# Optimization experiments

Hardware: AMD Instinct MI355X
Metric: run time of the kernel (lower is better)

Reference implementation:

```python
import jax, jax.numpy as jnp
import numpy as np

N_GRAPHS = 4
NODES_PER_GRAPH = 8192
N_NODES = N_GRAPHS * NODES_PER_GRAPH
N_EDGES = N_NODES * 16
IN_DIM = 3
HID = 128
K_OUT = 512
MAX_WAVELENGTH = 10000.0


def _glorot(k, shape):
    lim = (6.0 / (shape[0] + shape[1])) ** 0.5
    return jax.random.uniform(k, shape, jnp.float32, -lim, lim)


def setup_inputs() -> dict:
    key = jax.random.key(0)
    ks = jax.random.split(key, 12)
    z = lambda *s: jnp.zeros(s, jnp.float32)
    return {
        "x": jax.random.normal(ks[0], (N_NODES, IN_DIM), jnp.float32),
        "mesh_pos": jax.random.uniform(ks[1], (N_NODES, 2), jnp.float32),
        "mesh_edges": jax.random.randint(ks[2], (N_EDGES, 2), 0, N_NODES, jnp.int32),
        "batch_idx": jnp.arange(N_NODES, dtype=jnp.int32) // NODES_PER_GRAPH,
        "proj_w": _glorot(ks[3], (IN_DIM, HID)), "proj_b": z(HID),
        "msg_w1": _glorot(ks[4], (2 * HID, HID)), "msg_b1": z(HID),
        "msg_w2": _glorot(ks[5], (HID, HID)), "msg_b2": z(HID),
        "upd_w1": _glorot(ks[6], (2 * HID, HID)), "upd_b1": z(HID),
        "upd_w2": _glorot(ks[7], (HID, HID)), "upd_b2": z(HID),
        "pool_rel_w": _glorot(ks[8], (HID, 1)), "pool_rel_b": z(1),
        "pool_root_w": _glorot(ks[9], (HID, 1)),
    }


def _sincos_embed(pos):
    # ContinuousSincosEmbed: HID=128, ndim=2 -> 64 channels per coord dim, 32 freqs
    dim_per_ndim = HID // 2
    omega = 1.0 / MAX_WAVELENGTH ** (jnp.arange(0, dim_per_ndim, 2, dtype=jnp.float32) / dim_per_ndim)
    ang = pos[:, :, None] * omega  # [N, ndim, 32]
    emb = jnp.concatenate([jnp.sin(ang), jnp.cos(ang)], axis=-1)  # [N, ndim, 64]
    return emb.reshape(pos.shape[0], HID)


def reference(x, mesh_pos, mesh_edges, batch_idx, proj_w, proj_b,
              msg_w1, msg_b1, msg_w2, msg_b2, upd_w1, upd_b1, upd_w2, upd_b2,
              pool_rel_w, pool_rel_b, pool_root_w):
    src, dst = mesh_edges[:, 0], mesh_edges[:, 1]  # edge_index[0]=j(src), [1]=i(dst)
    h = x @ proj_w + proj_b + _sincos_embed(mesh_pos)
    cnt = jnp.maximum(jax.ops.segment_sum(jnp.ones((N_EDGES,), h.dtype), dst, num_segments=N_NODES), 1.0)
    # message passing layer (depth=1): message MLP on [x_i, x_j], scatter-mean, residual update MLP
    m_in = jnp.concatenate([h[dst], h[src]], axis=-1)  # [E, 2H]
    m = jax.nn.silu(m_in @ msg_w1 + msg_b1) @ msg_w2 + msg_b2
    agg = jax.ops.segment_sum(m, dst, num_segments=N_NODES) / cnt[:, None]
    h = h + (jax.nn.silu(jnp.concatenate([h, agg], axis=-1) @ upd_w1 + upd_b1) @ upd_w2 + upd_b2)
    # SAGPooling score: GraphConv(HID,1,aggr='mean'), tanh nonlinearity
    nagg = jax.ops.segment_sum(h[src], dst, num_segments=N_NODES) / cnt[:, None]
    score = jnp.tanh((nagg @ pool_rel_w + pool_rel_b + h @ pool_root_w)[:, 0])
    # fixed top-k per graph (batch_idx is contiguous blocks of NODES_PER_GRAPH)
    topv, topi = jax.lax.top_k(score.reshape(N_GRAPHS, NODES_PER_GRAPH), K_OUT)
    perm = (topi + jnp.arange(N_GRAPHS, dtype=topi.dtype)[:, None] * NODES_PER_GRAPH).reshape(-1)
    x_pool = h[perm] * topv.reshape(-1)[:, None]
    batch_pool = jnp.repeat(jnp.arange(N_GRAPHS, dtype=batch_idx.dtype), K_OUT)
    return x_pool, batch_pool
```

## Files before the change

kernel.cpp:

```cpp
#include <hip/hip_runtime.h>
#include <hip/hip_bf16.h>
#include <math.h>

#define N_NODESC 32768
#define N_EDGESC 524288
#define NPG 8192
#define KOUT 512

typedef unsigned short u16;
typedef unsigned int u32;
typedef unsigned long long u64;

__device__ __forceinline__ float siluf(float x) {
    return x / (1.f + __expf(-x));
}

__global__ __launch_bounds__(256) void k_h0(const float* __restrict__ x,
                                            const float* __restrict__ pos,
                                            const float* __restrict__ pw,
                                            const float* __restrict__ pb,
                                            float* __restrict__ h,
                                            int* __restrict__ deg) {
    int gid = blockIdx.x * 256 + threadIdx.x;
    if (gid < N_NODESC) deg[gid] = 0;
    int node = blockIdx.x * 2 + (threadIdx.x >> 7);
    int c = threadIdx.x & 127;
    float x0 = x[node * 3 + 0];
    float x1 = x[node * 3 + 1];
    float x2 = x[node * 3 + 2];
    float acc = x0 * pw[c] + x1 * pw[128 + c] + x2 * pw[256 + c];
    acc += pb[c];
    int dim = c >> 6;
    int inner = c & 63;
    int jj = inner & 31;
    float p = pos[node * 2 + dim];
    float omega = exp2f(-(float)jj * 0.41524101186092027f);
    float ang = p * omega;
    acc += (inner < 32) ? __sinf(ang) : __cosf(ang);
    h[(size_t)node * 128 + c] = acc;
}

__global__ __launch_bounds__(256) void k_deg(const int* __restrict__ edges, int* __restrict__ deg) {
    int e = blockIdx.x * 256 + threadIdx.x;
    if (e < N_EDGESC) {
        int2 e2 = ((const int2*)edges)[e];
        atomicAdd(&deg[e2.y], 1);
    }
}

__global__ __launch_bounds__(1024) void k_scan(const int* __restrict__ deg,
                                               int* __restrict__ off, int* __restrict__ cur,
                                               float* __restrict__ rs, float* __restrict__ bg) {
    __shared__ int ls[1024];
    int tid = threadIdx.x;
    int base = tid * 32;
    int v[32];
    int s = 0;
#pragma unroll
    for (int j = 0; j < 32; j++) { v[j] = deg[base + j]; s += v[j]; }
    ls[tid] = s;
    __syncthreads();
    for (int ofs = 1; ofs < 1024; ofs <<= 1) {
        int t = (tid >= ofs) ? ls[tid - ofs] : 0;
        __syncthreads();
        ls[tid] += t;
        __syncthreads();
    }
    int run = ls[tid] - s;
#pragma unroll
    for (int j = 0; j < 32; j++) {
        off[base + j] = run;
        cur[base + j] = run;
        int d = v[j];
        rs[base + j] = 1.f / (float)(d > 0 ? d : 1);
        bg[base + j] = d > 0 ? 1.f : 0.f;
        run += d;
    }
}

__global__ __launch_bounds__(256) void k_fill(const int* __restrict__ edges,
                                              int* __restrict__ cur, int* __restrict__ csr) {
    int e = blockIdx.x * 256 + threadIdx.x;
    if (e < N_EDGESC) {
        int2 e2 = ((const int2*)edges)[e];
        int pos = atomicAdd(&cur[e2.y], 1);
        csr[pos] = e2.x;
    }
}

__global__ __launch_bounds__(256) void k_sortcsr(int* __restrict__ csr,
                                                 const int* __restrict__ off,
                                                 const int* __restrict__ deg) {
    int d = blockIdx.x * 4 + (threadIdx.x >> 6);
    int lane = threadIdx.x & 63;
    int o = off[d], n = deg[d];
    if (n <= 1) return;
    if (n <= 64) {
        int key = (lane < n) ? csr[o + lane] : 0x7FFFFFFF;
        for (int k = 2; k <= 64; k <<= 1) {
            for (int j = k >> 1; j > 0; j >>= 1) {
                int partner = __shfl_xor(key, j);
                bool asc = ((lane & k) == 0);
                bool keepMin = (((lane & j) == 0) == asc);
                key = keepMin ? min(key, partner) : max(key, partner);
            }
        }
        if (lane < n) csr[o + lane] = key;
    } else {
        if (lane == 0) {
            for (int i = o + 1; i < o + n; i++) {
                int x = csr[i];
                int j = i - 1;
                while (j >= o && csr[j] > x) { csr[j + 1] = csr[j]; j--; }
                csr[j + 1] = x;
            }
        }
    }
}

__global__ __launch_bounds__(256, 2) void gemm_dualw(const float* __restrict__ A,
                                                     const float* __restrict__ Wv,
                                                     const float* __restrict__ Wu,
                                                     const float* __restrict__ bu,
                                                     float* __restrict__ V, float* __restrict__ U) {
    __shared__ float Wsv[32 * 128];
    __shared__ float Wsu[32 * 128];
    int tid = threadIdx.x;
    int cg = tid & 31;
    int rg = tid >> 5;
    int m0 = blockIdx.x * 32 + rg * 4;
    int c0 = cg * 4;
    const float* Ar = A + (size_t)m0 * 128;

    float accv[4][4], accu[4][4];
#pragma unroll
    for (int r = 0; r < 4; r++)
#pragma unroll
        for (int c = 0; c < 4; c++) { accv[r][c] = 0.f; accu[r][c] = 0.f; }

    for (int kc = 0; kc < 128; kc += 32) {
        __syncthreads();
        {
            const float4* Wgv = (const float4*)(Wv + (size_t)kc * 128);
            const float4* Wgu = (const float4*)(Wu + (size_t)kc * 128);
            float4* Wlv = (float4*)Wsv;
            float4* Wlu = (float4*)Wsu;
#pragma unroll
            for (int i = 0; i < 4; i++) {
                Wlv[tid + i * 256] = Wgv[tid + i * 256];
                Wlu[tid + i * 256] = Wgu[tid + i * 256];
            }
        }
        __syncthreads();
#pragma unroll
        for (int k0 = 0; k0 < 32; k0 += 4) {
            float4 a[4];
#pragma unroll
            for (int r = 0; r < 4; r++) a[r] = *(const float4*)(Ar + r * 128 + kc + k0);
#pragma unroll
            for (int kk = 0; kk < 4; kk++) {
                float4 wv = *(const float4*)(Wsv + (k0 + kk) * 128 + c0);
                float4 wu = *(const float4*)(Wsu + (k0 + kk) * 128 + c0);
#pragma unroll
                for (int r = 0; r < 4; r++) {
                    float aa = ((const float*)&a[r])[kk];
                    accv[r][0] += aa * wv.x; accv[r][1] += aa * wv.y;
                    accv[r][2] += aa * wv.z; accv[r][3] += aa * wv.w;
                    accu[r][0] += aa * wu.x; accu[r][1] += aa * wu.y;
                    accu[r][2] += aa * wu.z; accu[r][3] += aa * wu.w;
                }
            }
        }
    }
#pragma unroll
    for (int r = 0; r < 4; r++) {
        int row = m0 + r;
        float4 ov, ou;
        ov.x = accv[r][0]; ov.y = accv[r][1]; ov.z = accv[r][2]; ov.w = accv[r][3];
        ou.x = accu[r][0] + bu[c0];
        ou.y = accu[r][1] + bu[c0 + 1];
        ou.z = accu[r][2] + bu[c0 + 2];
        ou.w = accu[r][3] + bu[c0 + 3];
        *(float4*)(V + (size_t)row * 128 + c0) = ov;
        *(float4*)(U + (size_t)row * 128 + c0) = ou;
    }
}

__global__ __launch_bounds__(256, 2) void gemm_chain(const float* __restrict__ S,
                                                     float* __restrict__ h,
                                                     const float* __restrict__ W2,
                                                     const float* __restrict__ b2,
                                                     const float* __restrict__ rs,
                                                     const float* __restrict__ bg,
                                                     const float* __restrict__ U1a,
                                                     const float* __restrict__ U1b,
                                                     const float* __restrict__ ub1,
                                                     const float* __restrict__ U2,
                                                     const float* __restrict__ ub2,
                                                     const float* __restrict__ wrel,
                                                     const float* __restrict__ wroot,
                                                     float* __restrict__ pout,
                                                     float* __restrict__ rout) {
    __shared__ float Wc[32 * 128];
    __shared__ float T[32 * 128];
    int tid = threadIdx.x;
    int cg = tid & 31;
    int rg = tid >> 5;
    int m0 = blockIdx.x * 32 + rg * 4;
    int c0 = cg * 4;
    const float* Sr = S + (size_t)m0 * 128;
    const float* hr = h + (size_t)m0 * 128;

    float acc1[4][4], acc2[4][4];

#define ZERO(acc)                                                        \
    {                                                                    \
        _Pragma("unroll") for (int r = 0; r < 4; r++)                    \
            _Pragma("unroll") for (int c = 0; c < 4; c++) acc[r][c] = 0.f; \
    }
#define STAGE_W(Wsrc, kc)                                                \
    {                                                                    \
        __syncthreads();                                                 \
        const float4* Wg = (const float4*)((Wsrc) + (size_t)(kc) * 128); \
        float4* Wl = (float4*)Wc;                                        \
        _Pragma("unroll") for (int i = 0; i < 4; i++)                    \
            Wl[tid + i * 256] = Wg[tid + i * 256];                       \
        __syncthreads();                                                 \
    }
#define COMPUTE_G(acc, Abase, kc)                                        \
    {                                                                    \
        _Pragma("unroll") for (int k0 = 0; k0 < 32; k0 += 4) {           \
            float4 a[4];                                                 \
            _Pragma("unroll") for (int r = 0; r < 4; r++)                \
                a[r] = *(const float4*)((Abase) + r * 128 + (kc) + k0);  \
            _Pragma("unroll") for (int kk = 0; kk < 4; kk++) {           \
                float4 wv = *(const float4*)(Wc + (k0 + kk) * 128 + c0); \
                _Pragma("unroll") for (int r = 0; r < 4; r++) {          \
                    float aa = ((const float*)&a[r])[kk];                \
                    acc[r][0] += aa * wv.x; acc[r][1] += aa * wv.y;      \
                    acc[r][2] += aa * wv.z; acc[r][3] += aa * wv.w;      \
                }                                                        \
            }                                                            \
        }                                                                \
    }
#define COMPUTE_T(acc, kc)                                               \
    {                                                                    \
        _Pragma("unroll") for (int k0 = 0; k0 < 32; k0 += 4) {           \
            float4 a[4];                                                 \
            _Pragma("unroll") for (int r = 0; r < 4; r++)                \
                a[r] = *(const float4*)(T + (rg * 4 + r) * 128 + (kc) + k0); \
            _Pragma("unroll") for (int kk = 0; kk < 4; kk++) {           \
                float4 wv = *(const float4*)(Wc + (k0 + kk) * 128 + c0); \
                _Pragma("unroll") for (int r = 0; r < 4; r++) {          \
                    float aa = ((const float*)&a[r])[kk];                \
                    acc[r][0] += aa * wv.x; acc[r][1] += aa * wv.y;      \
                    acc[r][2] += aa * wv.z; acc[r][3] += aa * wv.w;      \
                }                                                        \
            }                                                            \
        }                                                                \
    }

    ZERO(acc1)
    for (int kc = 0; kc < 128; kc += 32) {
        STAGE_W(W2, kc)
        COMPUTE_G(acc1, Sr, kc)
    }
#pragma unroll
    for (int r = 0; r < 4; r++) {
        int row = m0 + r;
        float rsv = rs[row];
        float bgv = bg[row];
        float4 o;
        float* op = (float*)&o;
#pragma unroll
        for (int c = 0; c < 4; c++) {
            float xv = acc1[r][c];
            xv *= rsv;
            xv += b2[c0 + c] * bgv;
            op[c] = xv;
        }
        *(float4*)(T + (rg * 4 + r) * 128 + c0) = o;
    }
    __syncthreads();

    ZERO(acc1)
    for (int kc = 0; kc < 128; kc += 32) {
        STAGE_W(U1a, kc)
        COMPUTE_G(acc1, hr, kc)
    }
    ZERO(acc2)
    for (int kc = 0; kc < 128; kc += 32) {
        STAGE_W(U1b, kc)
        COMPUTE_T(acc2, kc)
    }
    __syncthreads();
#pragma unroll
    for (int r = 0; r < 4; r++) {
        float4 o;
        float* op = (float*)&o;
#pragma unroll
        for (int c = 0; c < 4; c++) {
            float xv = acc1[r][c];
            xv += acc2[r][c];
            xv += ub1[c0 + c];
            op[c] = siluf(xv);
        }
        *(float4*)(T + (rg * 4 + r) * 128 + c0) = o;
    }
    __syncthreads();

    ZERO(acc1)
    for (int kc = 0; kc < 128; kc += 32) {
        STAGE_W(U2, kc)
        COMPUTE_T(acc1, kc)
    }
    float prel[4], prot[4];
#pragma unroll
    for (int r = 0; r < 4; r++) {
        int row = m0 + r;
        float4 o;
        float* op = (float*)&o;
#pragma unroll
        for (int c = 0; c < 4; c++) {
            float xv = acc1[r][c];
            xv *= 1.f;
            xv += ub2[c0 + c] * 1.f;
            xv += hr[r * 128 + c0 + c];
            op[c] = xv;
        }
        prel[r] = op[0] * wrel[c0] + op[1] * wrel[c0 + 1] + op[2] * wrel[c0 + 2] + op[3] * wrel[c0 + 3];
        prot[r] = op[0] * wroot[c0] + op[1] * wroot[c0 + 1] + op[2] * wroot[c0 + 2] + op[3] * wroot[c0 + 3];
        *(float4*)(h + (size_t)row * 128 + c0) = o;
    }
#pragma unroll
    for (int r = 0; r < 4; r++) {
        float a = prel[r], b = prot[r];
#pragma unroll
        for (int m = 1; m < 32; m <<= 1) {
            a += __shfl_xor(a, m);
            b += __shfl_xor(b, m);
        }
        if (cg == 0) { pout[m0 + r] = a; rout[m0 + r] = b; }
    }
#undef ZERO
#undef STAGE_W
#undef COMPUTE_G
#undef COMPUTE_T
}

__global__ __launch_bounds__(256) void k_accum_S(const float* __restrict__ v,
                                                 const int* __restrict__ csr, const int* __restrict__ off,
                                                 const int* __restrict__ deg, float* S) {
    int d = blockIdx.x * 4 + (threadIdx.x >> 6);
    int lane = threadIdx.x & 63;
    int half = lane >> 5;
    int l32 = lane & 31;
    float* srow = S + (size_t)d * 128;
    float4 u = *(const float4*)(srow + l32 * 4);
    float4 a = {0.f, 0.f, 0.f, 0.f};
    int o = off[d], n = deg[d];
    for (int base = 0; base < n; base += 64) {
        int cnt = min(64, n - base);
        int sall = (lane < cnt) ? csr[o + base + lane] : 0;
        int j = 0;
        for (; j + 8 <= cnt; j += 8) {
            int s0 = __shfl(sall, j + 0 + half);
            int s1 = __shfl(sall, j + 2 + half);
            int s2 = __shfl(sall, j + 4 + half);
            int s3 = __shfl(sall, j + 6 + half);
            float4 v0 = *(const float4*)(v + (size_t)s0 * 128 + l32 * 4);
            float4 v1 = *(const float4*)(v + (size_t)s1 * 128 + l32 * 4);
            float4 v2 = *(const float4*)(v + (size_t)s2 * 128 + l32 * 4);
            float4 v3 = *(const float4*)(v + (size_t)s3 * 128 + l32 * 4);
            a.x += siluf(u.x + v0.x); a.y += siluf(u.y + v0.y);
            a.z += siluf(u.z + v0.z); a.w += siluf(u.w + v0.w);
            a.x += siluf(u.x + v1.x); a.y += siluf(u.y + v1.y);
            a.z += siluf(u.z + v1.z); a.w += siluf(u.w + v1.w);
            a.x += siluf(u.x + v2.x); a.y += siluf(u.y + v2.y);
            a.z += siluf(u.z + v2.z); a.w += siluf(u.w + v2.w);
            a.x += siluf(u.x + v3.x); a.y += siluf(u.y + v3.y);
            a.z += siluf(u.z + v3.z); a.w += siluf(u.w + v3.w);
        }
        for (; j < cnt; j += 2) {
            if (j + 1 < cnt) {
                int s = __shfl(sall, j + half);
                float4 vv = *(const float4*)(v + (size_t)s * 128 + l32 * 4);
                a.x += siluf(u.x + vv.x); a.y += siluf(u.y + vv.y);
                a.z += siluf(u.z + vv.z); a.w += siluf(u.w + vv.w);
            } else {
                int s = __shfl(sall, j);
                if (half == 0) {
                    float4 vv = *(const float4*)(v + (size_t)s * 128 + l32 * 4);
                    a.x += siluf(u.x + vv.x); a.y += siluf(u.y + vv.y);
                    a.z += siluf(u.z + vv.z); a.w += siluf(u.w + vv.w);
                }
            }
        }
    }
    float ox = __shfl(a.x, l32 + 32);
    float oy = __shfl(a.y, l32 + 32);
    float oz = __shfl(a.z, l32 + 32);
    float ow = __shfl(a.w, l32 + 32);
    if (half == 0) {
        float4 t;
        t.x = a.x + ox; t.y = a.y + oy; t.z = a.z + oz; t.w = a.w + ow;
        *(float4*)(srow + l32 * 4) = t;
    }
}

__global__ __launch_bounds__(256) void k_score(const float* __restrict__ p, const float* __restrict__ r,
                                               const int* __restrict__ csr, const int* __restrict__ off,
                                               const int* __restrict__ deg, const float* __restrict__ relb,
                                               float* __restrict__ score) {
    int d = blockIdx.x * 4 + (threadIdx.x >> 6);
    int lane = threadIdx.x & 63;
    int o = off[d], n = deg[d];
    float a = 0.f;
    for (int j = lane; j < n; j += 64) a += p[csr[o + j]];
    for (int m = 32; m > 0; m >>= 1) a += __shfl_xor(a, m);
    if (lane == 0) {
        float cnt = (float)(n > 0 ? n : 1);
        score[d] = tanhf(a / cnt + relb[0] + r[d]);
    }
}

__global__ __launch_bounds__(1024) void k_topk(const float* __restrict__ score, const float* __restrict__ h,
                                               float* __restrict__ out) {
    __shared__ u32 ms[NPG];
    __shared__ u32 hist[256];
    __shared__ u32 sbuf[1024];
    __shared__ u64 sel[KOUT];
    __shared__ float ordv[KOUT];
    __shared__ int ordi[KOUT];
    __shared__ u32 selCnt, sPrefix, sNeed, sB;

    int g = blockIdx.x;
    int tid = threadIdx.x;

    for (int i = tid; i < NPG; i += 1024) {
        u32 u = __float_as_uint(score[(size_t)g * NPG + i]);
        ms[i] = (u & 0x80000000u) ? ~u : (u | 0x80000000u);
    }
    if (tid == 0) { sNeed = KOUT; sPrefix = 0; selCnt = 0; }
    __syncthreads();

    for (int pass = 0; pass < 4; pass++) {
        int shift = 24 - pass * 8;
        if (tid < 256) hist[tid] = 0;
        __syncthreads();
        u32 pfx = sPrefix;
        for (int i = tid; i < NPG; i += 1024) {
            u32 v = ms[i];
            if (pass == 0 || (v >> (shift + 8)) == pfx)
                atomicAdd(&hist[(v >> shift) & 255u], 1u);
        }
        __syncthreads();
        if (tid < 256) sbuf[tid] = hist[tid];
        __syncthreads();
        for (int ofs = 1; ofs < 256; ofs <<= 1) {
            u32 t = 0;
            if (tid < 256 && tid + ofs < 256) t = sbuf[tid + ofs];
            __syncthreads();
            if (tid < 256) sbuf[tid] += t;
            __syncthreads();
        }
        u32 need = sNeed;
        if (tid < 256) {
            if (sbuf[tid] >= need && (tid == 255 || sbuf[tid + 1] < need)) sB = (u32)tid;
        }
        __syncthreads();
        if (tid == 0) {
            u32 B = sB;
            u32 above = (B == 255) ? 0u : sbuf[B + 1];
            sNeed = need - above;
            sPrefix = (sPrefix << 8) | B;
        }
        __syncthreads();
    }
    u32 T = sPrefix;
    u32 rTie = sNeed;

    int base = tid * 8;
    u32 lc = 0;
#pragma unroll
    for (int j = 0; j < 8; j++) lc += (ms[base + j] == T);
    __syncthreads();
    sbuf[tid] = lc;
    __syncthreads();
    u32 own = lc;
    for (int ofs = 1; ofs < 1024; ofs <<= 1) {
        u32 t = (tid >= ofs) ? sbuf[tid - ofs] : 0;
        __syncthreads();
        sbuf[tid] += t;
        __syncthreads();
    }
    u32 excl = sbuf[tid] - own;

#pragma unroll
    for (int j = 0; j < 8; j++) {
        int i = base + j;
        u32 v = ms[i];
        bool pick = (v > T) || ((v == T) && (excl < rTie));
        if (v == T) excl++;
        if (pick) {
            u32 slot = atomicAdd(&selCnt, 1u);
            sel[slot] = ((u64)v << 32) | (u32)(NPG - 1 - i);
        }
    }
    __syncthreads();

    if (tid < KOUT) {
        u64 mine = sel[tid];
        int rank = 0;
        for (int j = 0; j < KOUT; j++) rank += (sel[j] > mine);
        u32 v = (u32)(mine >> 32);
        int idx = NPG - 1 - (int)(mine & 0xFFFFFFFFu);
        u32 uu = (v & 0x80000000u) ? (v & 0x7FFFFFFFu) : ~v;
        ordv[rank] = __uint_as_float(uu);
        ordi[rank] = idx;
    }
    __syncthreads();

    for (int t = tid; t < KOUT * 128; t += 1024) {
        int r = t >> 7, c = t & 127;
        int node = g * NPG + ordi[r];
        out[((size_t)g * KOUT + r) * 128 + c] = h[(size_t)node * 128 + c] * ordv[r];
    }
    for (int t = tid; t < KOUT; t += 1024)
        out[(size_t)4 * KOUT * 128 + (size_t)g * KOUT + t] = (float)g;
}

extern "C" void kernel_launch(void* const* d_in, const int* in_sizes, int n_in,
                              void* d_out, int out_size, void* d_ws, size_t ws_size,
                              hipStream_t stream) {
    const float* x        = (const float*)d_in[0];
    const float* mesh_pos = (const float*)d_in[1];
    const int*   edges    = (const int*)d_in[2];
    const float* proj_w   = (const float*)d_in[4];
    const float* proj_b   = (const float*)d_in[5];
    const float* msg_w1   = (const float*)d_in[6];
    const float* msg_b1   = (const float*)d_in[7];
    const float* msg_w2   = (const float*)d_in[8];
    const float* msg_b2   = (const float*)d_in[9];
    const float* upd_w1   = (const float*)d_in[10];
    const float* upd_b1   = (const float*)d_in[11];
    const float* upd_w2   = (const float*)d_in[12];
    const float* upd_b2   = (const float*)d_in[13];
    const float* pool_rel_w  = (const float*)d_in[14];
    const float* pool_rel_b  = (const float*)d_in[15];
    const float* pool_root_w = (const float*)d_in[16];
    float* out = (float*)d_out;

    char* w = (char*)d_ws;
    float* h  = (float*)(w);
    float* v  = (float*)(w + (1ull << 24));
    float* S  = (float*)(w + (2ull << 24));
    char* sm  = w + (3ull << 24);
    int*   deg   = (int*)(sm);
    int*   off   = (int*)(sm + 131072);
    int*   cur   = (int*)(sm + 262144);
    float* rsA   = (float*)(sm + 393216);
    float* bgA   = (float*)(sm + 524288);
    float* pp    = (float*)(sm + 655360);
    float* rr    = (float*)(sm + 786432);
    float* score = (float*)(sm + 917504);
    int*   csr   = (int*)(sm + 1048576);

    k_h0<<<N_NODESC / 2, 256, 0, stream>>>(x, mesh_pos, proj_w, proj_b, h, deg);
    k_deg<<<N_EDGESC / 256, 256, 0, stream>>>(edges, deg);
    k_scan<<<1, 1024, 0, stream>>>(deg, off, cur, rsA, bgA);
    k_fill<<<N_EDGESC / 256, 256, 0, stream>>>(edges, cur, csr);
    k_sortcsr<<<N_NODESC / 4, 256, 0, stream>>>(csr, off, deg);

    gemm_dualw<<<1024, 256, 0, stream>>>(h, msg_w1 + 128 * 128, msg_w1, msg_b1, v, S);
    k_accum_S<<<N_NODESC / 4, 256, 0, stream>>>(v, csr, off, deg, S);
    gemm_chain<<<1024, 256, 0, stream>>>(S, h, msg_w2, msg_b2, rsA, bgA,
                                         upd_w1, upd_w1 + 128 * 128, upd_b1,
                                         upd_w2, upd_b2,
                                         pool_rel_w, pool_root_w, pp, rr);

    k_score<<<N_NODESC / 4, 256, 0, stream>>>(pp, rr, csr, off, deg, pool_rel_b, score);
    k_topk<<<4, 1024, 0, stream>>>(score, h, out);
}
```

Measured before the change: 386.6 us.

## Double-buffer weight tiles in GEMMs and rework edge gather to scalar lanes

Both GEMM kernels now keep two shared-memory weight buffers and stage the next K chunk while computing on the current one, which removes one of the two barriers per chunk. The dual-weight GEMM uses 16-row chunks so its shared-memory footprint stays the same, while gemm_chain doubles its Wc buffer, which raises LDS use and may lower occupancy. The k_accum_S gather changes from half-wave float4 loads to full-wave scalar loads covering two 64-float halves, with 8 neighbours in flight and no cross-half shuffle reduction at the end.

```diff
diff --git a/kernel.cpp b/kernel.cpp
--- a/kernel.cpp
+++ b/kernel.cpp
@@ -123,8 +123,8 @@
                                                      const float* __restrict__ Wu,
                                                      const float* __restrict__ bu,
                                                      float* __restrict__ V, float* __restrict__ U) {
-    __shared__ float Wsv[32 * 128];
-    __shared__ float Wsu[32 * 128];
+    __shared__ float Wsv[2][16 * 128];
+    __shared__ float Wsu[2][16 * 128];
     int tid = threadIdx.x;
     int cg = tid & 31;
     int rg = tid >> 5;
@@ -138,29 +138,33 @@
 #pragma unroll
         for (int c = 0; c < 4; c++) { accv[r][c] = 0.f; accu[r][c] = 0.f; }
 
-    for (int kc = 0; kc < 128; kc += 32) {
-        __syncthreads();
-        {
-            const float4* Wgv = (const float4*)(Wv + (size_t)kc * 128);
-            const float4* Wgu = (const float4*)(Wu + (size_t)kc * 128);
-            float4* Wlv = (float4*)Wsv;
-            float4* Wlu = (float4*)Wsu;
-#pragma unroll
-            for (int i = 0; i < 4; i++) {
-                Wlv[tid + i * 256] = Wgv[tid + i * 256];
-                Wlu[tid + i * 256] = Wgu[tid + i * 256];
-            }
-        }
-        __syncthreads();
-#pragma unroll
-        for (int k0 = 0; k0 < 32; k0 += 4) {
+#define STAGE_DW(buf, kc)                                                          \
+    {                                                                              \
+        const float4* Wgv = (const float4*)(Wv + (size_t)(kc) * 128);              \
+        const float4* Wgu = (const float4*)(Wu + (size_t)(kc) * 128);              \
+        float4* Wlv = (float4*)Wsv[buf];                                           \
+        float4* Wlu = (float4*)Wsu[buf];                                           \
+        _Pragma("unroll") for (int i = 0; i < 2; i++) {                            \
+            Wlv[tid + i * 256] = Wgv[tid + i * 256];                               \
+            Wlu[tid + i * 256] = Wgu[tid + i * 256];                               \
+        }                                                                          \
+    }
+
+    STAGE_DW(0, 0)
+    __syncthreads();
+    for (int c = 0; c < 8; c++) {
+        int buf = c & 1;
+        if (c + 1 < 8) STAGE_DW(buf ^ 1, (c + 1) * 16)
+        int kc = c * 16;
+#pragma unroll
+        for (int k0 = 0; k0 < 16; k0 += 4) {
             float4 a[4];
 #pragma unroll
             for (int r = 0; r < 4; r++) a[r] = *(const float4*)(Ar + r * 128 + kc + k0);
 #pragma unroll
             for (int kk = 0; kk < 4; kk++) {
-                float4 wv = *(const float4*)(Wsv + (k0 + kk) * 128 + c0);
-                float4 wu = *(const float4*)(Wsu + (k0 + kk) * 128 + c0);
+                float4 wv = *(const float4*)(Wsv[buf] + (k0 + kk) * 128 + c0);
+                float4 wu = *(const float4*)(Wsu[buf] + (k0 + kk) * 128 + c0);
 #pragma unroll
                 for (int r = 0; r < 4; r++) {
                     float aa = ((const float*)&a[r])[kk];
@@ -171,7 +175,9 @@
                 }
             }
         }
-    }
+        __syncthreads();
+    }
+#undef STAGE_DW
 #pragma unroll
     for (int r = 0; r < 4; r++) {
         int row = m0 + r;
@@ -201,7 +207,7 @@
                                                      const float* __restrict__ wroot,
                                                      float* __restrict__ pout,
                                                      float* __restrict__ rout) {
-    __shared__ float Wc[32 * 128];
+    __shared__ float Wc[2][32 * 128];
     __shared__ float T[32 * 128];
     int tid = threadIdx.x;
     int cg = tid & 31;
@@ -213,58 +219,75 @@
 
     float acc1[4][4], acc2[4][4];
 
-#define ZERO(acc)                                                        \
-    {                                                                    \
-        _Pragma("unroll") for (int r = 0; r < 4; r++)                    \
+#define ZERO(acc)                                                          \
+    {                                                                      \
+        _Pragma("unroll") for (int r = 0; r < 4; r++)                      \
             _Pragma("unroll") for (int c = 0; c < 4; c++) acc[r][c] = 0.f; \
     }
-#define STAGE_W(Wsrc, kc)                                                \
-    {                                                                    \
-        __syncthreads();                                                 \
-        const float4* Wg = (const float4*)((Wsrc) + (size_t)(kc) * 128); \
-        float4* Wl = (float4*)Wc;                                        \
-        _Pragma("unroll") for (int i = 0; i < 4; i++)                    \
-            Wl[tid + i * 256] = Wg[tid + i * 256];                       \
-        __syncthreads();                                                 \
-    }
-#define COMPUTE_G(acc, Abase, kc)                                        \
-    {                                                                    \
-        _Pragma("unroll") for (int k0 = 0; k0 < 32; k0 += 4) {           \
-            float4 a[4];                                                 \
-            _Pragma("unroll") for (int r = 0; r < 4; r++)                \
-                a[r] = *(const float4*)((Abase) + r * 128 + (kc) + k0);  \
-            _Pragma("unroll") for (int kk = 0; kk < 4; kk++) {           \
-                float4 wv = *(const float4*)(Wc + (k0 + kk) * 128 + c0); \
-                _Pragma("unroll") for (int r = 0; r < 4; r++) {          \
-                    float aa = ((const float*)&a[r])[kk];                \
-                    acc[r][0] += aa * wv.x; acc[r][1] += aa * wv.y;      \
-                    acc[r][2] += aa * wv.z; acc[r][3] += aa * wv.w;      \
-                }                                                        \
-            }                                                            \
-        }                                                                \
-    }
-#define COMPUTE_T(acc, kc)                                               \
-    {                                                                    \
-        _Pragma("unroll") for (int k0 = 0; k0 < 32; k0 += 4) {           \
-            float4 a[4];                                                 \
-            _Pragma("unroll") for (int r = 0; r < 4; r++)                \
+#define STAGE_W(buf, Wsrc, kc)                                             \
+    {                                                                      \
+        const float4* Wg = (const float4*)((Wsrc) + (size_t)(kc) * 128);   \
+        float4* Wl = (float4*)Wc[buf];                                     \
+        _Pragma("unroll") for (int i = 0; i < 4; i++)                      \
+            Wl[tid + i * 256] = Wg[tid + i * 256];                         \
+    }
+#define COMPUTE_G(acc, buf, Abase, kc)                                     \
+    {                                                                      \
+        _Pragma("unroll") for (int k0 = 0; k0 < 32; k0 += 4) {             \
+            float4 a[4];                                                   \
+            _Pragma("unroll") for (int r = 0; r < 4; r++)                  \
+                a[r] = *(const float4*)((Abase) + r * 128 + (kc) + k0);    \
+            _Pragma("unroll") for (int kk = 0; kk < 4; kk++) {             \
+                float4 wv = *(const float4*)(Wc[buf] + (k0 + kk) * 128 + c0); \
+                _Pragma("unroll") for (int r = 0; r < 4; r++) {            \
+                    float aa = ((const float*)&a[r])[kk];                  \
+                    acc[r][0] += aa * wv.x; acc[r][1] += aa * wv.y;        \
+                    acc[r][2] += aa * wv.z; acc[r][3] += aa * wv.w;        \
+                }                                                          \
+            }                                                              \
+        }                                                                  \
+    }
+#define COMPUTE_T(acc, buf, kc)                                            \
+    {                                                                      \
+        _Pragma("unroll") for (int k0 = 0; k0 < 32; k0 += 4) {             \
+            float4 a[4];                                                   \
+            _Pragma("unroll") for (int r = 0; r < 4; r++)                  \
                 a[r] = *(const float4*)(T + (rg * 4 + r) * 128 + (kc) + k0); \
-            _Pragma("unroll") for (int kk = 0; kk < 4; kk++) {           \
-                float4 wv = *(const float4*)(Wc + (k0 + kk) * 128 + c0); \
-                _Pragma("unroll") for (int r = 0; r < 4; r++) {          \
-                    float aa = ((const float*)&a[r])[kk];                \
-                    acc[r][0] += aa * wv.x; acc[r][1] += aa * wv.y;      \
-                    acc[r][2] += aa * wv.z; acc[r][3] += aa * wv.w;      \
-                }                                                        \
-            }                                                            \
-        }                                                                \
+            _Pragma("unroll") for (int kk = 0; kk < 4; kk++) {             \
+                float4 wv = *(const float4*)(Wc[buf] + (k0 + kk) * 128 + c0); \
+                _Pragma("unroll") for (int r = 0; r < 4; r++) {            \
+                    float aa = ((const float*)&a[r])[kk];                  \
+                    acc[r][0] += aa * wv.x; acc[r][1] += aa * wv.y;        \
+                    acc[r][2] += aa * wv.z; acc[r][3] += aa * wv.w;        \
+                }                                                          \
+            }                                                              \
+        }                                                                  \
+    }
+#define PASS_G(acc, Wsrc, Abase)                                           \
+    {                                                                      \
+        STAGE_W(0, Wsrc, 0)                                                \
+        __syncthreads();                                                   \
+        _Pragma("unroll") for (int c = 0; c < 4; c++) {                    \
+            int buf = c & 1;                                               \
+            if (c + 1 < 4) STAGE_W(buf ^ 1, Wsrc, (c + 1) * 32)            \
+            COMPUTE_G(acc, buf, Abase, c * 32)                             \
+            __syncthreads();                                               \
+        }                                                                  \
+    }
+#define PASS_T(acc, Wsrc)                                                  \
+    {                                                                      \
+        STAGE_W(0, Wsrc, 0)                                                \
+        __syncthreads();                                                   \
+        _Pragma("unroll") for (int c = 0; c < 4; c++) {                    \
+            int buf = c & 1;                                               \
+            if (c + 1 < 4) STAGE_W(buf ^ 1, Wsrc, (c + 1) * 32)            \
+            COMPUTE_T(acc, buf, c * 32)                                    \
+            __syncthreads();                                               \
+        }                                                                  \
     }
 
     ZERO(acc1)
-    for (int kc = 0; kc < 128; kc += 32) {
-        STAGE_W(W2, kc)
-        COMPUTE_G(acc1, Sr, kc)
-    }
+    PASS_G(acc1, W2, Sr)
 #pragma unroll
     for (int r = 0; r < 4; r++) {
         int row = m0 + r;
@@ -284,15 +307,9 @@
     __syncthreads();
 
     ZERO(acc1)
-    for (int kc = 0; kc < 128; kc += 32) {
-        STAGE_W(U1a, kc)
-        COMPUTE_G(acc1, hr, kc)
-    }
+    PASS_G(acc1, U1a, hr)
     ZERO(acc2)
-    for (int kc = 0; kc < 128; kc += 32) {
-        STAGE_W(U1b, kc)
-        COMPUTE_T(acc2, kc)
-    }
+    PASS_T(acc2, U1b)
     __syncthreads();
 #pragma unroll
     for (int r = 0; r < 4; r++) {
@@ -310,10 +327,7 @@
     __syncthreads();
 
     ZERO(acc1)
-    for (int kc = 0; kc < 128; kc += 32) {
-        STAGE_W(U2, kc)
-        COMPUTE_T(acc1, kc)
-    }
+    PASS_T(acc1, U2)
     float prel[4], prot[4];
 #pragma unroll
     for (int r = 0; r < 4; r++) {
@@ -346,6 +360,8 @@
 #undef STAGE_W
 #undef COMPUTE_G
 #undef COMPUTE_T
+#undef PASS_G
+#undef PASS_T
 }
 
 __global__ __launch_bounds__(256) void k_accum_S(const float* __restrict__ v,
@@ -353,59 +369,45 @@
                                                  const int* __restrict__ deg, float* S) {
     int d = blockIdx.x * 4 + (threadIdx.x >> 6);
     int lane = threadIdx.x & 63;
-    int half = lane >> 5;
-    int l32 = lane & 31;
     float* srow = S + (size_t)d * 128;
-    float4 u = *(const float4*)(srow + l32 * 4);
-    float4 a = {0.f, 0.f, 0.f, 0.f};
+    float u0 = srow[lane];
+    float u1 = srow[64 + lane];
+    float a0 = 0.f, a1 = 0.f;
     int o = off[d], n = deg[d];
     for (int base = 0; base < n; base += 64) {
         int cnt = min(64, n - base);
         int sall = (lane < cnt) ? csr[o + base + lane] : 0;
         int j = 0;
         for (; j + 8 <= cnt; j += 8) {
-            int s0 = __shfl(sall, j + 0 + half);
-            int s1 = __shfl(sall, j + 2 + half);
-            int s2 = __shfl(sall, j + 4 + half);
-            int s3 = __shfl(sall, j + 6 + half);
-            float4 v0 = *(const float4*)(v + (size_t)s0 * 128 + l32 * 4);
-            float4 v1 = *(const float4*)(v + (size_t)s1 * 128 + l32 * 4);
-            float4 v2 = *(const float4*)(v + (size_t)s2 * 128 + l32 * 4);
-            float4 v3 = *(const float4*)(v + (size_t)s3 * 128 + l32 * 4);
-            a.x += siluf(u.x + v0.x); a.y += siluf(u.y + v0.y);
-            a.z += siluf(u.z + v0.z); a.w += siluf(u.w + v0.w);
-            a.x += siluf(u.x + v1.x); a.y += siluf(u.y + v1.y);
-            a.z += siluf(u.z + v1.z); a.w += siluf(u.w + v1.w);
-            a.x += siluf(u.x + v2.x); a.y += siluf(u.y + v2.y);
-            a.z += siluf(u.z + v2.z); a.w += siluf(u.w + v2.w);
-            a.x += siluf(u.x + v3.x); a.y += siluf(u.y + v3.y);
-            a.z += siluf(u.z + v3.z); a.w += siluf(u.w + v3.w);
-        }
-        for (; j < cnt; j += 2) {
-            if (j + 1 < cnt) {
-                int s = __shfl(sall, j + half);
-                float4 vv = *(const float4*)(v + (size_t)s * 128 + l32 * 4);
-                a.x += siluf(u.x + vv.x); a.y += siluf(u.y + vv.y);
-                a.z += siluf(u.z + vv.z); a.w += siluf(u.w + vv.w);
-            } else {
-                int s = __shfl(sall, j);
-                if (half == 0) {
-                    float4 vv = *(const float4*)(v + (size_t)s * 128 + l32 * 4);
-                    a.x += siluf(u.x + vv.x); a.y += siluf(u.y + vv.y);
-                    a.z += siluf(u.z + vv.z); a.w += siluf(u.w + vv.w);
-                }
-            }
-        }
-    }
-    float ox = __shfl(a.x, l32 + 32);
-    float oy = __shfl(a.y, l32 + 32);
-    float oz = __shfl(a.z, l32 + 32);
-    float ow = __shfl(a.w, l32 + 32);
-    if (half == 0) {
-        float4 t;
-        t.x = a.x + ox; t.y = a.y + oy; t.z = a.z + oz; t.w = a.w + ow;
-        *(float4*)(srow + l32 * 4) = t;
-    }
+            int s0 = __shfl(sall, j + 0), s1 = __shfl(sall, j + 1);
+            int s2 = __shfl(sall, j + 2), s3 = __shfl(sall, j + 3);
+            int s4 = __shfl(sall, j + 4), s5 = __shfl(sall, j + 5);
+            int s6 = __shfl(sall, j + 6), s7 = __shfl(sall, j + 7);
+            float v00 = v[(size_t)s0 * 128 + lane], v01 = v[(size_t)s0 * 128 + 64 + lane];
+            float v10 = v[(size_t)s1 * 128 + lane], v11 = v[(size_t)s1 * 128 + 64 + lane];
+            float v20 = v[(size_t)s2 * 128 + lane], v21 = v[(size_t)s2 * 128 + 64 + lane];
+            float v30 = v[(size_t)s3 * 128 + lane], v31 = v[(size_t)s3 * 128 + 64 + lane];
+            float v40 = v[(size_t)s4 * 128 + lane], v41 = v[(size_t)s4 * 128 + 64 + lane];
+            float v50 = v[(size_t)s5 * 128 + lane], v51 = v[(size_t)s5 * 128 + 64 + lane];
+            float v60 = v[(size_t)s6 * 128 + lane], v61 = v[(size_t)s6 * 128 + 64 + lane];
+            float v70 = v[(size_t)s7 * 128 + lane], v71 = v[(size_t)s7 * 128 + 64 + lane];
+            a0 += siluf(u0 + v00); a1 += siluf(u1 + v01);
+            a0 += siluf(u0 + v10); a1 += siluf(u1 + v11);
+            a0 += siluf(u0 + v20); a1 += siluf(u1 + v21);
+            a0 += siluf(u0 + v30); a1 += siluf(u1 + v31);
+            a0 += siluf(u0 + v40); a1 += siluf(u1 + v41);
+            a0 += siluf(u0 + v50); a1 += siluf(u1 + v51);
+            a0 += siluf(u0 + v60); a1 += siluf(u1 + v61);
+            a0 += siluf(u0 + v70); a1 += siluf(u1 + v71);
+        }
+        for (; j < cnt; j++) {
+            int s = __shfl(sall, j);
+            a0 += siluf(u0 + v[(size_t)s * 128 + lane]);
+            a1 += siluf(u1 + v[(size_t)s * 128 + 64 + lane]);
+        }
+    }
+    srow[lane] = a0;
+    srow[64 + lane] = a1;
 }
 
 __global__ __launch_bounds__(256) void k_score(const float* __restrict__ p, const float* __restrict__ r,
```

After: 374.6 us. -3.1%, faster.
